# Kernel tuning notes

Measured on AMD Instinct MI355X. Metric: run time of the kernel, lower is better.

The kernel has to match this reference:

```python
import jax, jax.numpy as jnp
import numpy as np

VOCAB, EMB, HID = 32000, 512, 1024
SEQ, BATCH = 512, 64


def _lstm_scan(x_seq, Wih, Whh, bih, bhh):
    """Run an LSTMCell over time. x_seq: [T, B, E]. Returns (hs, cs): [T, B, H].
    Gate order matches torch.nn.LSTMCell: i, f, g, o."""
    H = Whh.shape[1]
    B = x_seq.shape[1]
    # Precompute input projections for all timesteps in one big GEMM.
    x_proj = jnp.einsum('tbe,ge->tbg', x_seq, Wih) + bih  # [T, B, 4H]

    def step(carry, xp):
        h, c = carry
        gates = xp + h @ Whh.T + bhh  # [B, 4H]
        i, f, g, o = jnp.split(gates, 4, axis=-1)
        i = jax.nn.sigmoid(i)
        f = jax.nn.sigmoid(f)
        g = jnp.tanh(g)
        o = jax.nn.sigmoid(o)
        c = f * c + i * g
        h = o * jnp.tanh(c)
        return (h, c), (h, c)

    h0 = jnp.zeros((B, H), dtype=x_seq.dtype)
    c0 = jnp.zeros((B, H), dtype=x_seq.dtype)
    _, (hs, cs) = jax.lax.scan(step, (h0, c0), x_proj)
    return hs, cs


def setup_inputs() -> dict:
    key = jax.random.key(0)
    ks = jax.random.split(key, 10)
    s = 1.0 / np.sqrt(HID)
    u = lambda k, shape: jax.random.uniform(k, shape, jnp.float32, -s, s)
    source = jax.random.randint(ks[0], (SEQ, BATCH), 0, VOCAB)
    emb_w = jax.random.normal(ks[1], (VOCAB, EMB), jnp.float32)
    return {
        'source': source,
        'emb_w': emb_w,
        'Wih_f': u(ks[2], (4 * HID, EMB)),
        'Whh_f': u(ks[3], (4 * HID, HID)),
        'bih_f': u(ks[4], (4 * HID,)),
        'bhh_f': u(ks[5], (4 * HID,)),
        'Wih_b': u(ks[6], (4 * HID, EMB)),
        'Whh_b': u(ks[7], (4 * HID, HID)),
        'bih_b': u(ks[8], (4 * HID,)),
        'bhh_b': u(ks[9], (4 * HID,)),
    }


def reference(source, emb_w, Wih_f, Whh_f, bih_f, bhh_f, Wih_b, Whh_b, bih_b, bhh_b):
    # padding_idx=0: row 0 of the embedding is zero.
    emb_w = emb_w.at[0].set(0.0)
    embed = jnp.take(emb_w, source, axis=0)  # [T, B, E]
    # Forward direction.
    hs_f, cs_f = _lstm_scan(embed, Wih_f, Whh_f, bih_f, bhh_f)
    # Backward direction: run on reversed sequence, then flip back to align.
    hs_b_rev, cs_b_rev = _lstm_scan(embed[::-1], Wih_b, Whh_b, bih_b, bhh_b)
    hs_b = hs_b_rev[::-1]
    # hs[i] = hs_f[i] + hs_b[i], stacked along dim=1 -> [B, T, H]
    hs = jnp.transpose(hs_f + hs_b, (1, 0, 2))
    return hs
```

## Files before the change

kernel.cpp:

```cpp
#include <hip/hip_runtime.h>

#define TC 32
#define NCHUNK 16

typedef __attribute__((ext_vector_type(8))) short short8;
typedef __attribute__((ext_vector_type(4))) float float4_t;
typedef __attribute__((ext_vector_type(4))) unsigned int uint4_t;
typedef __attribute__((ext_vector_type(4))) unsigned short ushort4_t;

__device__ inline unsigned short f2bf(float f) {
  union { float f; unsigned u; } v; v.f = f;
  return (unsigned short)((v.u + 0x7fffu + ((v.u >> 16) & 1u)) >> 16);
}
__device__ inline float bf2f(unsigned short b) {
  union { unsigned u; float f; } v; v.u = ((unsigned)b) << 16;
  return v.f;
}
__device__ inline float sigmoidf_(float x) { return 1.f / (1.f + __expf(-x)); }
__device__ inline float tanhf_(float x) {
  float e = __expf(-2.f * fabsf(x));
  float t = (1.f - e) / (1.f + e);
  return x < 0.f ? -t : t;
}

__global__ __launch_bounds__(256)
void k_cvt2(const float* __restrict__ a, const float* __restrict__ b,
            unsigned short* __restrict__ o, unsigned halfElems) {
  const size_t i = ((size_t)blockIdx.x * 256 + threadIdx.x) * 8;
  const float* s = (i < (size_t)halfElems) ? (a + i) : (b + (i - halfElems));
  float4_t x = *(const float4_t*)s;
  float4_t y = *(const float4_t*)(s + 4);
  short8 v;
  v[0]=(short)f2bf(x.x); v[1]=(short)f2bf(x.y); v[2]=(short)f2bf(x.z); v[3]=(short)f2bf(x.w);
  v[4]=(short)f2bf(y.x); v[5]=(short)f2bf(y.y); v[6]=(short)f2bf(y.z); v[7]=(short)f2bf(y.w);
  *(short8*)(o + i) = v;
}

__global__ __launch_bounds__(256)
void k_embed_c(const int* __restrict__ src, const float* __restrict__ emb,
               unsigned short* __restrict__ o, int rowF0, int rowB0) {
  const int wi = blockIdx.x * 4 + (threadIdx.x >> 6);
  const int lane = threadIdx.x & 63;
  const int half = wi >> 11;
  const int rl = wi & 2047;
  const int row = (half ? rowB0 : rowF0) + rl;
  const int tok = src[row];
  short8 v;
  if (tok == 0) {
    v = (short8){0,0,0,0,0,0,0,0};
  } else {
    const float* ep = emb + (size_t)tok * 512 + lane * 8;
    float4_t a = *(const float4_t*)(ep);
    float4_t b = *(const float4_t*)(ep + 4);
    v[0]=(short)f2bf(a.x); v[1]=(short)f2bf(a.y); v[2]=(short)f2bf(a.z); v[3]=(short)f2bf(a.w);
    v[4]=(short)f2bf(b.x); v[5]=(short)f2bf(b.y); v[6]=(short)f2bf(b.z); v[7]=(short)f2bf(b.w);
  }
  *(short8*)(o + ((size_t)half * 2048 + rl) * 512 + lane * 8) = v;
}

__global__ __launch_bounds__(256, 2)
void k_xproj(const unsigned short* __restrict__ Aall,
             const unsigned short* __restrict__ Ball,
             const float* __restrict__ bih_f, const float* __restrict__ bhh_f,
             const float* __restrict__ bih_b, const float* __restrict__ bhh_b,
             unsigned short* __restrict__ xp) {
  __shared__ __align__(16) unsigned short lA[128 * 64];
  __shared__ __align__(16) unsigned short lB[128 * 64];
  const int tid = threadIdx.x;
  const int lane = tid & 63;
  const int w = tid >> 6;
  const int mq = w & 1, nq = w >> 1;
  const int half = blockIdx.x >> 9;
  const int idx = blockIdx.x & 511;
  const int bm = idx & 15;
  const int bn = idx >> 4;
  const unsigned short* A  = Aall + (size_t)half * 1048576;
  const unsigned short* Bw = Ball + (size_t)half * 2097152;

  float4_t acc[4][4];
#pragma unroll
  for (int i = 0; i < 4; ++i)
#pragma unroll
    for (int j = 0; j < 4; ++j) acc[i][j] = (float4_t){0.f, 0.f, 0.f, 0.f};

  for (int kc = 0; kc < 8; ++kc) {
    __syncthreads();
#pragma unroll
    for (int i = 0; i < 4; ++i) {
      const int r = i * 32 + (tid >> 3);
      const int g = tid & 7;
      const int p = g ^ (r & 7);
      uint4_t va = *(const uint4_t*)(A + (size_t)(bm * 128 + r) * 512 + kc * 64 + g * 8);
      *(uint4_t*)&lA[r * 64 + p * 8] = va;
      uint4_t vb = *(const uint4_t*)(Bw + (size_t)(bn * 128 + r) * 512 + kc * 64 + g * 8);
      *(uint4_t*)&lB[r * 64 + p * 8] = vb;
    }
    __syncthreads();
#pragma unroll
    for (int ks = 0; ks < 2; ++ks) {
      short8 af[4], bf[4];
#pragma unroll
      for (int i = 0; i < 4; ++i) {
        const int m = mq * 64 + i * 16 + (lane & 15);
        const int blkm = ((lane >> 4) + 4 * ks) ^ (m & 7);
        af[i] = *(const short8*)&lA[m * 64 + blkm * 8];
        const int n = nq * 64 + i * 16 + (lane & 15);
        const int blkn = ((lane >> 4) + 4 * ks) ^ (n & 7);
        bf[i] = *(const short8*)&lB[n * 64 + blkn * 8];
      }
#pragma unroll
      for (int i = 0; i < 4; ++i)
#pragma unroll
        for (int j = 0; j < 4; ++j)
          acc[i][j] = __builtin_amdgcn_mfma_f32_16x16x32_bf16(af[i], bf[j], acc[i][j], 0, 0, 0);
    }
  }
  float biasj[4];
#pragma unroll
  for (int j = 0; j < 4; ++j) {
    const int n = bn * 128 + nq * 64 + j * 16 + (lane & 15);
    biasj[j] = half ? (bih_b[n] + bhh_b[n]) : (bih_f[n] + bhh_f[n]);
  }
#pragma unroll
  for (int i = 0; i < 4; ++i) {
    const int mt = bm * 8 + mq * 4 + i;
#pragma unroll
    for (int j = 0; j < 4; ++j) {
      const int nt = bn * 8 + nq * 4 + j;
      ushort4_t o;
      o.x = f2bf(acc[i][j].x + biasj[j]);
      o.y = f2bf(acc[i][j].y + biasj[j]);
      o.z = f2bf(acc[i][j].z + biasj[j]);
      o.w = f2bf(acc[i][j].w + biasj[j]);
      *(ushort4_t*)(xp + (size_t)half * 8388608 + ((size_t)mt * 256 + nt) * 256 + lane * 4) = o;
    }
  }
}

__global__ __launch_bounds__(256)
void k_step(const unsigned short* __restrict__ xp,
            const unsigned short* __restrict__ whh_b,
            unsigned short* __restrict__ h_buf,
            float* __restrict__ c_state,
            float* __restrict__ out,
            int s) {
  __shared__ __align__(16) unsigned short hS[64 * 256];
  __shared__ float gbuf[4096];
  const int tid = threadIdx.x;
  const int lane = tid & 63;
  const int gt = tid >> 6;
  const int dir = blockIdx.x >> 6;
  const int cg = blockIdx.x & 63;
  const int t = dir ? (511 - s) : s;

  const int mtlbase = (dir ? (31 - (s & 31)) : (s & 31)) * 4;
  const int ntl = gt * 64 + cg;
  float4_t acc[4];
#pragma unroll
  for (int mt = 0; mt < 4; ++mt) {
    ushort4_t xpv = *(const ushort4_t*)(xp + (size_t)dir * 8388608 +
                                        ((size_t)(mtlbase + mt) * 256 + ntl) * 256 + lane * 4);
    acc[mt] = (float4_t){bf2f(xpv.x), bf2f(xpv.y), bf2f(xpv.z), bf2f(xpv.w)};
  }

  const unsigned short* hbase = h_buf + (size_t)(dir * 2 + ((s + 1) & 1)) * 65536;
  const unsigned short* wrow = whh_b + (size_t)dir * 4194304 +
      (size_t)(gt * 1024 + cg * 16 + (lane & 15)) * 1024 + (lane >> 4) * 8;
  const int sr = tid >> 2;
  const int sg = tid & 3;
  const int mrow = lane & 15;

  for (int kc = 0; kc < 4; ++kc) {
    short8 bf[8];
#pragma unroll
    for (int ks = 0; ks < 8; ++ks) bf[ks] = *(const short8*)(wrow + kc * 256 + ks * 32);
    uint4_t hv[8];
#pragma unroll
    for (int i = 0; i < 8; ++i) {
      const int g = sg + 4 * i;
      hv[i] = *(const uint4_t*)(hbase + (size_t)sr * 1024 + kc * 256 + g * 8);
    }
    if (kc) __syncthreads();
#pragma unroll
    for (int i = 0; i < 8; ++i) {
      const int g = sg + 4 * i;
      *(uint4_t*)&hS[sr * 256 + ((g ^ (sr & 31)) * 8)] = hv[i];
    }
    __syncthreads();
#pragma unroll
    for (int ks = 0; ks < 8; ++ks) {
#pragma unroll
      for (int mt = 0; mt < 4; ++mt) {
        const int m = mt * 16 + mrow;
        const int phys = (ks * 4 + (lane >> 4)) ^ (m & 31);
        short8 a = *(const short8*)&hS[m * 256 + phys * 8];
        acc[mt] = __builtin_amdgcn_mfma_f32_16x16x32_bf16(a, bf[ks], acc[mt], 0, 0, 0);
      }
    }
  }

#pragma unroll
  for (int mt = 0; mt < 4; ++mt) {
#pragma unroll
    for (int r = 0; r < 4; ++r) {
      float v = acc[mt][r];
      v = (gt == 2) ? tanhf_(v) : sigmoidf_(v);
      gbuf[gt * 1024 + (mt * 16 + (lane >> 4) * 4 + r) * 16 + (lane & 15)] = v;
    }
  }
  __syncthreads();

  {
    const int b = tid >> 2;
    const int cb = (tid & 3) * 4;
    float4_t ig = *(float4_t*)&gbuf[b * 16 + cb];
    float4_t fg = *(float4_t*)&gbuf[1024 + b * 16 + cb];
    float4_t gg = *(float4_t*)&gbuf[2048 + b * 16 + cb];
    float4_t og = *(float4_t*)&gbuf[3072 + b * 16 + cb];
    float* cp = c_state + (size_t)dir * 65536 + (size_t)b * 1024 + cg * 16 + cb;
    float4_t c = *(float4_t*)cp;
    c.x = fg.x * c.x + ig.x * gg.x;
    c.y = fg.y * c.y + ig.y * gg.y;
    c.z = fg.z * c.z + ig.z * gg.z;
    c.w = fg.w * c.w + ig.w * gg.w;
    *(float4_t*)cp = c;
    float4_t hvv;
    hvv.x = og.x * tanhf_(c.x);
    hvv.y = og.y * tanhf_(c.y);
    hvv.z = og.z * tanhf_(c.z);
    hvv.w = og.w * tanhf_(c.w);
    ushort4_t hb;
    hb.x = f2bf(hvv.x); hb.y = f2bf(hvv.y); hb.z = f2bf(hvv.z); hb.w = f2bf(hvv.w);
    *(ushort4_t*)(h_buf + (size_t)(dir * 2 + (s & 1)) * 65536 +
                  (size_t)b * 1024 + cg * 16 + cb) = hb;
    float* op = out + ((size_t)b * 512 + t) * 1024 + cg * 16 + cb;
    const bool first = (dir == 0) == (t < 256);
    if (first) {
      *(float4_t*)op = hvv;
    } else {
      float4_t o = *(float4_t*)op;
      o.x += hvv.x; o.y += hvv.y; o.z += hvv.z; o.w += hvv.w;
      *(float4_t*)op = o;
    }
  }
}

extern "C" void kernel_launch(void* const* d_in, const int* in_sizes, int n_in,
                              void* d_out, int out_size, void* d_ws, size_t ws_size,
                              hipStream_t stream) {
  const int*   src  = (const int*)d_in[0];
  const float* emb  = (const float*)d_in[1];
  const float* WihF = (const float*)d_in[2];
  const float* WhhF = (const float*)d_in[3];
  const float* bihF = (const float*)d_in[4];
  const float* bhhF = (const float*)d_in[5];
  const float* WihB = (const float*)d_in[6];
  const float* WhhB = (const float*)d_in[7];
  const float* bihB = (const float*)d_in[8];
  const float* bhhB = (const float*)d_in[9];
  float* out = (float*)d_out;
  char* ws = (char*)d_ws;

  unsigned short* wih_b   = (unsigned short*)(ws);
  unsigned short* whh_b   = (unsigned short*)(ws + 8388608ull);
  unsigned short* embed_c = (unsigned short*)(ws + 25165824ull);
  unsigned short* xp      = (unsigned short*)(ws + 29360128ull);
  unsigned short* hbuf    = (unsigned short*)(ws + 62914560ull);
  float*          cstate  = (float*)         (ws + 63438848ull);

  hipMemsetAsync(hbuf, 0, 1048576ull, stream);
  k_cvt2<<<2048, 256, 0, stream>>>(WihF, WihB, wih_b, 4096u * 512u);
  k_cvt2<<<4096, 256, 0, stream>>>(WhhF, WhhB, whh_b, 4096u * 1024u);

  for (int ch = 0; ch < NCHUNK; ++ch) {
    const int tF0 = ch * TC;
    const int tB0 = 512 - TC - ch * TC;
    k_embed_c<<<1024, 256, 0, stream>>>(src, emb, embed_c, tF0 * 64, tB0 * 64);
    k_xproj<<<1024, 256, 0, stream>>>(embed_c, wih_b, bihF, bhhF, bihB, bhhB, xp);
    for (int sl = 0; sl < TC; ++sl) {
      k_step<<<128, 256, 0, stream>>>(xp, whh_b, hbuf, cstate, out, ch * TC + sl);
    }
  }
}
```

Baseline: 5.954 ms.

## Fuse per-chunk LSTM steps into a persistent cooperative kernel with LDS-resident weights

Replaces the 32 per-timestep k_step launches per chunk with one cooperative kernel that loops over the 32 steps and separates them with grid.sync(). Each block loads its 64x1024 slice of Whh into LDS once per chunk (128KB) instead of re-reading it from global memory every step. The cell state is also kept in registers across steps. The intent is to remove launch overhead and the repeated weight traffic. In exchange it pays grid-wide barrier latency and uses a large LDS footprint that limits occupancy to one block per CU.

```diff
diff --git a/kernel.cpp b/kernel.cpp
--- a/kernel.cpp
+++ b/kernel.cpp
@@ -1,4 +1,7 @@
 #include <hip/hip_runtime.h>
+#include <hip/hip_cooperative_groups.h>
+
+namespace cg = cooperative_groups;
 
 #define TC 32
 #define NCHUNK 16
@@ -138,111 +141,142 @@
 }
 
 __global__ __launch_bounds__(256)
-void k_step(const unsigned short* __restrict__ xp,
-            const unsigned short* __restrict__ whh_b,
-            unsigned short* __restrict__ h_buf,
-            float* __restrict__ c_state,
-            float* __restrict__ out,
-            int s) {
-  __shared__ __align__(16) unsigned short hS[64 * 256];
-  __shared__ float gbuf[4096];
+void k_steps32(const unsigned short* __restrict__ xp,
+               const unsigned short* __restrict__ whh_b,
+               unsigned short* __restrict__ h_buf,
+               float* __restrict__ c_state,
+               float* __restrict__ out,
+               int s0) {
+  __shared__ __align__(16) unsigned short wS[64 * 1024];
+  __shared__ __align__(16) float sgbuf[4096];
+  unsigned short* hS = (unsigned short*)sgbuf;
+  float* gbuf = sgbuf;
+
   const int tid = threadIdx.x;
   const int lane = tid & 63;
   const int gt = tid >> 6;
   const int dir = blockIdx.x >> 6;
-  const int cg = blockIdx.x & 63;
-  const int t = dir ? (511 - s) : s;
-
-  const int mtlbase = (dir ? (31 - (s & 31)) : (s & 31)) * 4;
-  const int ntl = gt * 64 + cg;
-  float4_t acc[4];
-#pragma unroll
-  for (int mt = 0; mt < 4; ++mt) {
-    ushort4_t xpv = *(const ushort4_t*)(xp + (size_t)dir * 8388608 +
-                                        ((size_t)(mtlbase + mt) * 256 + ntl) * 256 + lane * 4);
-    acc[mt] = (float4_t){bf2f(xpv.x), bf2f(xpv.y), bf2f(xpv.z), bf2f(xpv.w)};
-  }
-
-  const unsigned short* hbase = h_buf + (size_t)(dir * 2 + ((s + 1) & 1)) * 65536;
-  const unsigned short* wrow = whh_b + (size_t)dir * 4194304 +
-      (size_t)(gt * 1024 + cg * 16 + (lane & 15)) * 1024 + (lane >> 4) * 8;
+  const int cgi = blockIdx.x & 63;
+
+  {
+    const unsigned short* wbase = whh_b + (size_t)dir * 4194304;
+#pragma unroll
+    for (int g = 0; g < 4; ++g) {
+      const unsigned short* gb = wbase + (size_t)(g * 1024 + cgi * 16) * 1024;
+#pragma unroll
+      for (int i = 0; i < 8; ++i) {
+        const int uf = i * 256 + tid;
+        const int r = uf >> 7;
+        const int u = uf & 127;
+        uint4_t v = *(const uint4_t*)(gb + (size_t)r * 1024 + u * 8);
+        const int lr = g * 16 + r;
+        const int phys = (u & 96) | ((u & 31) ^ (lr & 31));
+        *(uint4_t*)&wS[(lr * 128 + phys) * 8] = v;
+      }
+    }
+  }
+
+  const int eb = tid >> 2;
+  const int ecb = (tid & 3) * 4;
+  float* cp = c_state + (size_t)dir * 65536 + (size_t)eb * 1024 + cgi * 16 + ecb;
+  float4_t creg = *(float4_t*)cp;
+
+  cg::grid_group grid = cg::this_grid();
+  __syncthreads();
+
   const int sr = tid >> 2;
   const int sg = tid & 3;
   const int mrow = lane & 15;
-
-  for (int kc = 0; kc < 4; ++kc) {
-    short8 bf[8];
-#pragma unroll
-    for (int ks = 0; ks < 8; ++ks) bf[ks] = *(const short8*)(wrow + kc * 256 + ks * 32);
-    uint4_t hv[8];
-#pragma unroll
-    for (int i = 0; i < 8; ++i) {
-      const int g = sg + 4 * i;
-      hv[i] = *(const uint4_t*)(hbase + (size_t)sr * 1024 + kc * 256 + g * 8);
-    }
-    if (kc) __syncthreads();
-#pragma unroll
-    for (int i = 0; i < 8; ++i) {
-      const int g = sg + 4 * i;
-      *(uint4_t*)&hS[sr * 256 + ((g ^ (sr & 31)) * 8)] = hv[i];
-    }
+  const int ntl = gt * 64 + cgi;
+
+  for (int sl = 0; sl < TC; ++sl) {
+    const int s = s0 + sl;
+    const int t = dir ? (511 - s) : s;
+    const int mtlbase = (dir ? (31 - sl) : sl) * 4;
+
+    float4_t acc[4];
+#pragma unroll
+    for (int mt = 0; mt < 4; ++mt) {
+      ushort4_t xpv = *(const ushort4_t*)(xp + (size_t)dir * 8388608 +
+                                          ((size_t)(mtlbase + mt) * 256 + ntl) * 256 + lane * 4);
+      acc[mt] = (float4_t){bf2f(xpv.x), bf2f(xpv.y), bf2f(xpv.z), bf2f(xpv.w)};
+    }
+
+    const unsigned short* hbase = h_buf + (size_t)(dir * 2 + ((s + 1) & 1)) * 65536;
+
+    for (int kc = 0; kc < 8; ++kc) {
+      uint4_t hv[4];
+#pragma unroll
+      for (int i = 0; i < 4; ++i) {
+        hv[i] = *(const uint4_t*)(hbase + (size_t)sr * 1024 + kc * 128 + (sg + 4 * i) * 8);
+      }
+      if (kc) __syncthreads();
+#pragma unroll
+      for (int i = 0; i < 4; ++i) {
+        const int g = sg + 4 * i;
+        *(uint4_t*)&hS[(sr * 16 + (g ^ (sr & 15))) * 8] = hv[i];
+      }
+      __syncthreads();
+#pragma unroll
+      for (int ks = 0; ks < 4; ++ks) {
+        const int lrB = gt * 16 + mrow;
+        const int u = kc * 16 + ks * 4 + (lane >> 4);
+        const int physB = (u & 96) | ((u & 31) ^ (lrB & 31));
+        short8 bfr = *(const short8*)&wS[(lrB * 128 + physB) * 8];
+#pragma unroll
+        for (int mt = 0; mt < 4; ++mt) {
+          const int m = mt * 16 + mrow;
+          const int ua = ks * 4 + (lane >> 4);
+          short8 a = *(const short8*)&hS[(m * 16 + (ua ^ (m & 15))) * 8];
+          acc[mt] = __builtin_amdgcn_mfma_f32_16x16x32_bf16(a, bfr, acc[mt], 0, 0, 0);
+        }
+      }
+    }
+
     __syncthreads();
-#pragma unroll
-    for (int ks = 0; ks < 8; ++ks) {
-#pragma unroll
-      for (int mt = 0; mt < 4; ++mt) {
-        const int m = mt * 16 + mrow;
-        const int phys = (ks * 4 + (lane >> 4)) ^ (m & 31);
-        short8 a = *(const short8*)&hS[m * 256 + phys * 8];
-        acc[mt] = __builtin_amdgcn_mfma_f32_16x16x32_bf16(a, bf[ks], acc[mt], 0, 0, 0);
-      }
-    }
-  }
-
-#pragma unroll
-  for (int mt = 0; mt < 4; ++mt) {
-#pragma unroll
-    for (int r = 0; r < 4; ++r) {
-      float v = acc[mt][r];
-      v = (gt == 2) ? tanhf_(v) : sigmoidf_(v);
-      gbuf[gt * 1024 + (mt * 16 + (lane >> 4) * 4 + r) * 16 + (lane & 15)] = v;
-    }
-  }
-  __syncthreads();
-
-  {
-    const int b = tid >> 2;
-    const int cb = (tid & 3) * 4;
-    float4_t ig = *(float4_t*)&gbuf[b * 16 + cb];
-    float4_t fg = *(float4_t*)&gbuf[1024 + b * 16 + cb];
-    float4_t gg = *(float4_t*)&gbuf[2048 + b * 16 + cb];
-    float4_t og = *(float4_t*)&gbuf[3072 + b * 16 + cb];
-    float* cp = c_state + (size_t)dir * 65536 + (size_t)b * 1024 + cg * 16 + cb;
-    float4_t c = *(float4_t*)cp;
-    c.x = fg.x * c.x + ig.x * gg.x;
-    c.y = fg.y * c.y + ig.y * gg.y;
-    c.z = fg.z * c.z + ig.z * gg.z;
-    c.w = fg.w * c.w + ig.w * gg.w;
-    *(float4_t*)cp = c;
-    float4_t hvv;
-    hvv.x = og.x * tanhf_(c.x);
-    hvv.y = og.y * tanhf_(c.y);
-    hvv.z = og.z * tanhf_(c.z);
-    hvv.w = og.w * tanhf_(c.w);
-    ushort4_t hb;
-    hb.x = f2bf(hvv.x); hb.y = f2bf(hvv.y); hb.z = f2bf(hvv.z); hb.w = f2bf(hvv.w);
-    *(ushort4_t*)(h_buf + (size_t)(dir * 2 + (s & 1)) * 65536 +
-                  (size_t)b * 1024 + cg * 16 + cb) = hb;
-    float* op = out + ((size_t)b * 512 + t) * 1024 + cg * 16 + cb;
-    const bool first = (dir == 0) == (t < 256);
-    if (first) {
-      *(float4_t*)op = hvv;
-    } else {
-      float4_t o = *(float4_t*)op;
-      o.x += hvv.x; o.y += hvv.y; o.z += hvv.z; o.w += hvv.w;
-      *(float4_t*)op = o;
-    }
-  }
+
+#pragma unroll
+    for (int mt = 0; mt < 4; ++mt) {
+#pragma unroll
+      for (int r = 0; r < 4; ++r) {
+        float v = acc[mt][r];
+        v = (gt == 2) ? tanhf_(v) : sigmoidf_(v);
+        gbuf[gt * 1024 + (mt * 16 + (lane >> 4) * 4 + r) * 16 + mrow] = v;
+      }
+    }
+    __syncthreads();
+
+    {
+      float4_t ig = *(float4_t*)&gbuf[eb * 16 + ecb];
+      float4_t fg = *(float4_t*)&gbuf[1024 + eb * 16 + ecb];
+      float4_t gg = *(float4_t*)&gbuf[2048 + eb * 16 + ecb];
+      float4_t og = *(float4_t*)&gbuf[3072 + eb * 16 + ecb];
+      creg.x = fg.x * creg.x + ig.x * gg.x;
+      creg.y = fg.y * creg.y + ig.y * gg.y;
+      creg.z = fg.z * creg.z + ig.z * gg.z;
+      creg.w = fg.w * creg.w + ig.w * gg.w;
+      float4_t hvv;
+      hvv.x = og.x * tanhf_(creg.x);
+      hvv.y = og.y * tanhf_(creg.y);
+      hvv.z = og.z * tanhf_(creg.z);
+      hvv.w = og.w * tanhf_(creg.w);
+      ushort4_t hb;
+      hb.x = f2bf(hvv.x); hb.y = f2bf(hvv.y); hb.z = f2bf(hvv.z); hb.w = f2bf(hvv.w);
+      *(ushort4_t*)(h_buf + (size_t)(dir * 2 + (s & 1)) * 65536 +
+                    (size_t)eb * 1024 + cgi * 16 + ecb) = hb;
+      float* op = out + ((size_t)eb * 512 + t) * 1024 + cgi * 16 + ecb;
+      const bool first = (dir == 0) == (t < 256);
+      if (first) {
+        *(float4_t*)op = hvv;
+      } else {
+        float4_t o = *(float4_t*)op;
+        o.x += hvv.x; o.y += hvv.y; o.z += hvv.z; o.w += hvv.w;
+        *(float4_t*)op = o;
+      }
+    }
+    if (sl < TC - 1) grid.sync();
+  }
+  *(float4_t*)cp = creg;
 }
 
 extern "C" void kernel_launch(void* const* d_in, const int* in_sizes, int n_in,
@@ -277,8 +311,9 @@
     const int tB0 = 512 - TC - ch * TC;
     k_embed_c<<<1024, 256, 0, stream>>>(src, emb, embed_c, tF0 * 64, tB0 * 64);
     k_xproj<<<1024, 256, 0, stream>>>(embed_c, wih_b, bihF, bhhF, bihB, bhhB, xp);
-    for (int sl = 0; sl < TC; ++sl) {
-      k_step<<<128, 256, 0, stream>>>(xp, whh_b, hbuf, cstate, out, ch * TC + sl);
-    }
-  }
-}
+    int s0 = ch * TC;
+    void* args[] = {(void*)&xp, (void*)&whh_b, (void*)&hbuf, (void*)&cstate,
+                    (void*)&out, (void*)&s0};
+    hipLaunchCooperativeKernel(k_steps32, dim3(128), dim3(256), args, 0u, stream);
+  }
+}
```

After: 12.37 ms. +107.8%, slower.
